# Kernel optimization log

Hardware: AMD Instinct MI355X
Metric: run time of the kernel (lower is better)

The kernel has to match this reference:

```python
import jax, jax.numpy as jnp
import numpy as np

NPOINT = 1024
K = 16
D_MODEL = 512
EPS = 1e-5


def _fps(xyz, npoint):
    # deterministic farthest point sampling (start at index 0)
    B, N, _ = xyz.shape
    def step(carry, _):
        dist, far = carry                                   # [B,N], [B]
        cent = jnp.take_along_axis(xyz, far[:, None, None], axis=1)  # [B,1,3]
        d = jnp.sum((xyz - cent) ** 2, axis=-1)             # [B,N]
        dist = jnp.minimum(dist, d)
        nxt = jnp.argmax(dist, axis=-1).astype(jnp.int32)
        return (dist, nxt), far
    init = (jnp.full((B, N), 1e10, xyz.dtype), jnp.zeros((B,), jnp.int32))
    _, idx = jax.lax.scan(step, init, None, length=npoint)
    return jnp.transpose(idx)                                # [B, npoint]


def _bn_relu(x, gamma, beta):
    # BatchNorm (training-mode batch stats, biased var) over all axes but channel-last
    axes = tuple(range(x.ndim - 1))
    mu = jnp.mean(x, axes, keepdims=True)
    var = jnp.var(x, axes, keepdims=True)
    return jax.nn.relu((x - mu) * jax.lax.rsqrt(var + EPS) * gamma + beta)


def _forward(xyz, feat, w1, b1, g1, bt1, fc1_w, fc1_b, wq, wk, wv, fc2_w, fc2_b,
             w2, b2, g2, bt2):
    B, N, C = feat.shape
    fps_idx = _fps(xyz, NPOINT)                              # [B,S]
    new_xyz = jnp.take_along_axis(xyz, fps_idx[:, :, None], axis=1)  # [B,S,3]
    # kNN of sampled centers against all points: squared distances [B,S,N]
    d = (jnp.sum(new_xyz ** 2, -1)[:, :, None]
         + jnp.sum(xyz ** 2, -1)[:, None, :]
         - 2.0 * jnp.einsum('bsc,bnc->bsn', new_xyz, xyz))
    _, knn_idx = jax.lax.top_k(-d, K)                        # [B,S,K]
    grouped = jnp.take_along_axis(
        feat, knn_idx.reshape(B, -1)[:, :, None], axis=1
    ).reshape(B, NPOINT, K, C)                               # [B,S,K,C]
    # mlp1: 1x1 conv + BN + ReLU (channel-last)
    x = _bn_relu(grouped @ w1.T + b1, g1, bt1)
    # TransformerBlock: local self-attention over the K neighbors
    pre = x
    h = x @ fc1_w.T + fc1_b                                  # [B,S,K,D]
    q, kk, v = h @ wq.T, h @ wk.T, h @ wv.T
    attn = jax.nn.softmax(
        jnp.einsum('bsnd,bsmd->bsnm', q, kk) / np.sqrt(D_MODEL), axis=-1)
    res = jnp.einsum('bsnm,bsmd->bsnd', attn, v)
    x = res @ fc2_w.T + fc2_b + pre                          # [B,S,K,C]
    # mlp2: 1x1 conv + BN + ReLU -> out_channel
    x = _bn_relu(x @ w2.T + b2, g2, bt2)                     # [B,S,K,out]
    new_feat = jnp.max(x, axis=2)                            # max-pool over neighbors
    return new_xyz, new_feat


def setup_inputs() -> dict:
    key = jax.random.key(0)
    ks = jax.random.split(key, 12)
    s = 0.02
    return {
        'xyz': jax.random.uniform(ks[0], (8, 4096, 3), jnp.float32),
        'feat': jax.random.normal(ks[1], (8, 4096, 64), jnp.float32),
        'w1': jax.random.normal(ks[2], (64, 64), jnp.float32) * s,
        'b1': jnp.zeros((64,), jnp.float32),
        'g1': jnp.ones((64,), jnp.float32),
        'bt1': jnp.zeros((64,), jnp.float32),
        'fc1_w': jax.random.normal(ks[3], (512, 64), jnp.float32) * s,
        'fc1_b': jnp.zeros((512,), jnp.float32),
        'wq': jax.random.normal(ks[4], (512, 512), jnp.float32) * s,
        'wk': jax.random.normal(ks[5], (512, 512), jnp.float32) * s,
        'wv': jax.random.normal(ks[6], (512, 512), jnp.float32) * s,
        'fc2_w': jax.random.normal(ks[7], (64, 512), jnp.float32) * s,
        'fc2_b': jnp.zeros((64,), jnp.float32),
        'w2': jax.random.normal(ks[8], (128, 64), jnp.float32) * s,
        'b2': jnp.zeros((128,), jnp.float32),
        'g2': jnp.ones((128,), jnp.float32),
        'bt2': jnp.zeros((128,), jnp.float32),
    }


def reference(xyz, feat, w1, b1, g1, bt1, fc1_w, fc1_b, wq, wk, wv, fc2_w, fc2_b,
              w2, b2, g2, bt2):
    return _forward(xyz, feat, w1, b1, g1, bt1, fc1_w, fc1_b, wq, wk, wv,
                    fc2_w, fc2_b, w2, b2, g2, bt2)
```

## Files before the change

### kernel.cpp

```cpp
#include <hip/hip_runtime.h>

#define EPSBN 1e-5f
#define INVSQ 0.04419417382415922f

#define WS_KNN_IDX   32768u
#define WS_X1        1048576u
#define WS_BNP1      34603008u
#define WS_BN1S      34865152u
#define WS_BNP2      34865664u
#define WS_BN2S      35914240u
#define WS_A         35915264u
#define WS_B         36046336u
#define WS_QB        36177408u
#define WS_KB        36179456u
#define WS_WC        36181504u
#define WS_G         36312576u
#define WS_ZT        36328960u
#define WS_U         36345344u
#define WS_W         36345600u
#define WS_TB        36345856u
#define WS_CC        36346112u
#define WS_PTS4      36346368u

__global__ __launch_bounds__(256) void prep1_kernel(const float* __restrict__ wq,
                                                    const float* __restrict__ wk,
                                                    const float* __restrict__ fc1w,
                                                    const float* __restrict__ fc1b,
                                                    const float* __restrict__ fc2w,
                                                    const float* __restrict__ wv,
                                                    const float* __restrict__ xyz,
                                                    float* __restrict__ A, float* __restrict__ B,
                                                    float* __restrict__ qb, float* __restrict__ kb,
                                                    float* __restrict__ Wc,
                                                    float4* __restrict__ pts4) {
  const int blk = blockIdx.x;
  if (blk < 256) {
    int id = blk * 256 + threadIdx.x;
    int which = id >> 15;
    int rem = id & 32767;
    int r = rem >> 6, i = rem & 63;
    const float* W = which ? wk : wq;
    float s = 0.f;
    for (int d = 0; d < 512; ++d) s = fmaf(W[r * 512 + d], fc1w[d * 64 + i], s);
    (which ? B : A)[r * 64 + i] = s;
    if (i == 0) {
      float sb = 0.f;
      for (int d = 0; d < 512; ++d) sb = fmaf(W[r * 512 + d], fc1b[d], sb);
      (which ? kb : qb)[r] = sb;
    }
  } else if (blk < 384) {
    int id = (blk - 256) * 256 + threadIdx.x;
    int c = id >> 9, d = id & 511;
    float s = 0.f;
    for (int e = 0; e < 512; ++e) s = fmaf(fc2w[c * 512 + e], wv[e * 512 + d], s);
    Wc[c * 512 + d] = s;
  } else {
    int id = (blk - 384) * 256 + threadIdx.x;
    float x = xyz[id * 3 + 0], y = xyz[id * 3 + 1], z = xyz[id * 3 + 2];
    float pp = __fadd_rn(__fadd_rn(__fmul_rn(x, x), __fmul_rn(y, y)), __fmul_rn(z, z));
    pts4[id] = make_float4(x, y, z, pp);
  }
}

#define FPS_REDSTEP(CTRL)                                                              \
  {                                                                                    \
    unsigned lo2 = (unsigned)__builtin_amdgcn_update_dpp(0, (int)klo, CTRL, 0xF, 0xF, true); \
    unsigned hi2 = (unsigned)__builtin_amdgcn_update_dpp(0, (int)khi, CTRL, 0xF, 0xF, true); \
    bool tk = (hi2 > khi) || (hi2 == khi && lo2 > klo);                                \
    khi = tk ? hi2 : khi; klo = tk ? lo2 : klo;                                        \
  }

__global__ __launch_bounds__(256) void fps_prep2_kernel(
    const float4* __restrict__ pts4, float* __restrict__ out_xyz,
    const float* __restrict__ A, const float* __restrict__ B,
    const float* __restrict__ qb, const float* __restrict__ kb,
    const float* __restrict__ Wc, const float* __restrict__ fc1w,
    const float* __restrict__ fc1b, const float* __restrict__ fc2b,
    float* __restrict__ G, float* __restrict__ u, float* __restrict__ w,
    float* __restrict__ cc, float* __restrict__ ZT, float* __restrict__ tb) {
  if (blockIdx.x >= 8) {
    const int blk = blockIdx.x - 8;
    if (blk < 17) {
      int id = blk * 256 + threadIdx.x;
      if (id < 4096) {
        int i = id >> 6, j = id & 63;
        float s = 0.f;
        for (int d = 0; d < 512; ++d) s = fmaf(A[d * 64 + i], B[d * 64 + j], s);
        G[i * 64 + j] = s * INVSQ;
      } else if (id < 4160) {
        int i = id - 4096; float s = 0.f;
        for (int d = 0; d < 512; ++d) s = fmaf(A[d * 64 + i], kb[d], s);
        u[i] = s * INVSQ;
      } else if (id < 4224) {
        int j = id - 4160; float s = 0.f;
        for (int d = 0; d < 512; ++d) s = fmaf(B[d * 64 + j], qb[d], s);
        w[j] = s * INVSQ;
      } else if (id == 4224) {
        float s = 0.f;
        for (int d = 0; d < 512; ++d) s = fmaf(qb[d], kb[d], s);
        cc[0] = s * INVSQ;
      }
    } else {
      int id = (blk - 17) * 256 + threadIdx.x;
      if (id < 4096) {
        int i = id >> 6, c = id & 63;
        float s = 0.f;
        for (int d = 0; d < 512; ++d) s = fmaf(Wc[c * 512 + d], fc1w[d * 64 + i], s);
        ZT[i * 64 + c] = s;
      } else if (id < 4160) {
        int c = id - 4096; float s = 0.f;
        for (int d = 0; d < 512; ++d) s = fmaf(Wc[c * 512 + d], fc1b[d], s);
        tb[c] = s + fc2b[c];
      }
    }
    return;
  }
  __shared__ float4 spts[4096];
  __shared__ float4 cent4[1024];
  __shared__ unsigned long long red[2][4];
  const int b = blockIdx.x;
  const int t = threadIdx.x;
  const int lane = t & 63, wid = t >> 6;
  const float4* pb = pts4 + (size_t)b * 4096;
  float px[16], py[16], pz[16], pd[16];
#pragma unroll
  for (int i = 0; i < 16; ++i) {
    int j = i * 256 + t;
    float4 p = pb[j];
    spts[j] = p;
    px[i] = p.x; py[i] = p.y; pz[i] = p.z; pd[i] = 1e10f;
  }
  __syncthreads();
  float4 c4 = spts[0];
  for (int it = 0; it < 1024; ++it) {
    if (t == 0) cent4[it] = c4;
    float bv = -1.0f; int bj = 0;
#pragma unroll
    for (int i = 0; i < 16; ++i) {
      float dx = __fsub_rn(px[i], c4.x);
      float dy = __fsub_rn(py[i], c4.y);
      float dz = __fsub_rn(pz[i], c4.z);
      float d = __fadd_rn(__fadd_rn(__fmul_rn(dx, dx), __fmul_rn(dy, dy)), __fmul_rn(dz, dz));
      float nd = fminf(pd[i], d);
      pd[i] = nd;
      bool g = nd > bv;
      bv = g ? nd : bv;
      bj = g ? (i * 256 + t) : bj;
    }
    unsigned klo = 4095u - (unsigned)bj;
    unsigned khi = __float_as_uint(bv);
    FPS_REDSTEP(0x111)
    FPS_REDSTEP(0x112)
    FPS_REDSTEP(0x114)
    FPS_REDSTEP(0x118)
    FPS_REDSTEP(0x142)
    FPS_REDSTEP(0x143)
    unsigned wlo = (unsigned)__builtin_amdgcn_readlane((int)klo, 63);
    unsigned whi = (unsigned)__builtin_amdgcn_readlane((int)khi, 63);
    const int par = it & 1;
    if (lane == 0) red[par][wid] = (((unsigned long long)whi) << 32) | wlo;
    __syncthreads();
    const ulonglong2* r2 = reinterpret_cast<const ulonglong2*>(&red[par][0]);
    ulonglong2 ka = r2[0];
    ulonglong2 kb2 = r2[1];
    unsigned long long m0 = (ka.x > ka.y) ? ka.x : ka.y;
    unsigned long long m1 = (kb2.x > kb2.y) ? kb2.x : kb2.y;
    unsigned long long k0 = (m0 > m1) ? m0 : m1;
    int jw = 4095 - (int)(unsigned)(k0 & 0xFFFFFFFFull);
    c4 = spts[jw];
  }
  __syncthreads();
  for (int o = t; o < 3072; o += 256) {
    int j = o / 3;
    int c = o - 3 * j;
    out_xyz[(size_t)b * 3072 + o] = (&cent4[j].x)[c];
  }
}

__global__ __launch_bounds__(256) void knn_kernel(const float4* __restrict__ pts4,
                                                  const float* __restrict__ new_xyz,
                                                  int* __restrict__ knn_idx) {
  const int t = threadIdx.x & 63;
  const int wave = (blockIdx.x << 2) | (threadIdx.x >> 6);
  const int b = wave >> 10;
  const float4* P = pts4 + (size_t)b * 4096;
  const float cx = new_xyz[(size_t)wave * 3 + 0];
  const float cy = new_xyz[(size_t)wave * 3 + 1];
  const float cz = new_xyz[(size_t)wave * 3 + 2];
  const float cc = __fadd_rn(__fadd_rn(__fmul_rn(cx, cx), __fmul_rn(cy, cy)), __fmul_rn(cz, cz));
  float ldd[16]; int ldi[16];
#pragma unroll
  for (int q = 0; q < 16; ++q) { ldd[q] = 3.4e38f; ldi[q] = 0x7fffffff; }
  for (int i = 0; i < 64; ++i) {
    int j = i * 64 + t;
    float4 p = P[j];
    float dot = __fadd_rn(__fadd_rn(__fmul_rn(cx, p.x), __fmul_rn(cy, p.y)), __fmul_rn(cz, p.z));
    float d = __fsub_rn(__fadd_rn(cc, p.w), __fmul_rn(2.0f, dot));
    if (d < ldd[15] || (d == ldd[15] && j < ldi[15])) {
      float cd = d; int ci = j;
#pragma unroll
      for (int q = 0; q < 16; ++q) {
        bool sw = (cd < ldd[q]) || (cd == ldd[q] && ci < ldi[q]);
        float td = ldd[q]; int ti = ldi[q];
        if (sw) { ldd[q] = cd; ldi[q] = ci; cd = td; ci = ti; }
      }
    }
  }
  float cd = ldd[0]; int ci = ldi[0];
  int* op = knn_idx + (size_t)wave * 16;
#pragma unroll 1
  for (int k = 0; k < 16; ++k) {
    float wd = cd; int wi = ci;
#pragma unroll
    for (int off = 1; off < 64; off <<= 1) {
      float ov = __shfl_xor(wd, off);
      int   oi = __shfl_xor(wi, off);
      bool tk = (ov < wd) || (ov == wd && oi < wi);
      wd = tk ? ov : wd; wi = tk ? oi : wi;
    }
    if (t == 0) op[k] = wi;
    if (wd == cd && wi == ci) {
#pragma unroll
      for (int q = 0; q < 15; ++q) { ldd[q] = ldd[q + 1]; ldi[q] = ldi[q + 1]; }
      ldd[15] = 3.4e38f; ldi[15] = 0x7fffffff;
    }
    cd = ldd[0]; ci = ldi[0];
  }
}

__global__ __launch_bounds__(256) void mlp1_kernel(const float* __restrict__ feat,
                                                   const int* __restrict__ knn_idx,
                                                   const float* __restrict__ w1,
                                                   const float* __restrict__ b1,
                                                   float* __restrict__ x1,
                                                   float* __restrict__ bnp1) {
  __shared__ float w1s[64 * 64];
  __shared__ float b1s[64];
  __shared__ float ls[4][64], lq[4][64];
  const int t = threadIdx.x;
  for (int i = t; i < 4096; i += 256) w1s[i] = w1[i];
  if (t < 64) b1s[t] = b1[t];
  __syncthreads();
  const int pos = blockIdx.x * 256 + t;
  const int b = pos >> 14;
  const int n = knn_idx[pos];
  const float4* fp = reinterpret_cast<const float4*>(feat + ((size_t)(b * 4096 + n)) * 64);
  float4 fr[16];
#pragma unroll
  for (int i = 0; i < 16; ++i) fr[i] = fp[i];
  float4* op = reinterpret_cast<float4*>(x1 + (size_t)pos * 64);
#pragma unroll
  for (int cq = 0; cq < 16; ++cq) {
    float a0 = b1s[cq * 4 + 0], a1 = b1s[cq * 4 + 1], a2 = b1s[cq * 4 + 2], a3 = b1s[cq * 4 + 3];
#pragma unroll
    for (int iq = 0; iq < 16; ++iq) {
      float4 f4 = fr[iq];
      float4 wa = *reinterpret_cast<const float4*>(&w1s[(cq * 4 + 0) * 64 + iq * 4]);
      float4 wb = *reinterpret_cast<const float4*>(&w1s[(cq * 4 + 1) * 64 + iq * 4]);
      float4 wc = *reinterpret_cast<const float4*>(&w1s[(cq * 4 + 2) * 64 + iq * 4]);
      float4 wd = *reinterpret_cast<const float4*>(&w1s[(cq * 4 + 3) * 64 + iq * 4]);
      a0 += f4.x * wa.x + f4.y * wa.y + f4.z * wa.z + f4.w * wa.w;
      a1 += f4.x * wb.x + f4.y * wb.y + f4.z * wb.z + f4.w * wb.w;
      a2 += f4.x * wc.x + f4.y * wc.y + f4.z * wc.z + f4.w * wc.w;
      a3 += f4.x * wd.x + f4.y * wd.y + f4.z * wd.z + f4.w * wd.w;
    }
    op[cq] = make_float4(a0, a1, a2, a3);
  }
  __threadfence_block();
  __syncthreads();
  {
    const int c2 = t & 63, g = t >> 6;
    const float* p = x1 + ((size_t)blockIdx.x * 256 + g * 64) * 64 + c2;
    float s = 0.f, s2 = 0.f;
    for (int i = 0; i < 64; ++i) { float v = p[(size_t)i * 64]; s += v; s2 = fmaf(v, v, s2); }
    ls[g][c2] = s; lq[g][c2] = s2;
  }
  __syncthreads();
  if (t < 64) {
    bnp1[blockIdx.x * 128 + t]      = ls[0][t] + ls[1][t] + ls[2][t] + ls[3][t];
    bnp1[blockIdx.x * 128 + 64 + t] = lq[0][t] + lq[1][t] + lq[2][t] + lq[3][t];
  }
}

__global__ __launch_bounds__(256) void bn1_final_kernel(const float* __restrict__ bnp1,
                                                        const float* __restrict__ g1,
                                                        const float* __restrict__ bt1,
                                                        float* __restrict__ bn1s) {
  __shared__ float rs[4][64], rq[4][64];
  const int t = threadIdx.x, c = t & 63, g = t >> 6;
  float S = 0.f, Q = 0.f;
  for (int i = g * 128; i < g * 128 + 128; ++i) {
    S += bnp1[i * 128 + c];
    Q += bnp1[i * 128 + 64 + c];
  }
  rs[g][c] = S; rq[g][c] = Q;
  __syncthreads();
  if (t < 64) {
    float Sa = rs[0][t] + rs[1][t] + rs[2][t] + rs[3][t];
    float Qa = rq[0][t] + rq[1][t] + rq[2][t] + rq[3][t];
    float m = Sa * (1.0f / 131072.0f);
    float var = Qa * (1.0f / 131072.0f) - m * m;
    float sc = g1[t] * rsqrtf(var + EPSBN);
    bn1s[t] = sc;
    bn1s[64 + t] = bt1[t] - m * sc;
  }
}

__global__ __launch_bounds__(64) void transformer_fused(
    float* __restrict__ x1, const float* __restrict__ bn1s,
    const float* __restrict__ G, const float* __restrict__ u, const float* __restrict__ w,
    const float* __restrict__ cc, const float* __restrict__ ZT, const float* __restrict__ tb) {
  __shared__ float pre[16][65];
  __shared__ float ts[16][65];
  __shared__ float ys[16][65];
  __shared__ float ss[16][17];
  __shared__ float spu[16], spw[16];
  const int c = threadIdx.x;
  const size_t base = (size_t)blockIdx.x * 1024;
  const float sc = bn1s[c], sh = bn1s[64 + c];
  float pc[16];
#pragma unroll
  for (int k = 0; k < 16; ++k) {
    float v = x1[base + k * 64 + c];
    float p = fmaxf(0.f, v * sc + sh);
    pc[k] = p; pre[k][c] = p;
  }
  __syncthreads();
  float tcol[16], ycol[16];
#pragma unroll
  for (int k = 0; k < 16; ++k) { tcol[k] = 0.f; ycol[k] = 0.f; }
  for (int i = 0; i < 64; ++i) {
    float g = G[i * 64 + c];
    float z = ZT[i * 64 + c];
#pragma unroll
    for (int k = 0; k < 16; ++k) {
      float p = pre[k][i];
      tcol[k] = fmaf(p, g, tcol[k]);
      ycol[k] = fmaf(p, z, ycol[k]);
    }
  }
#pragma unroll
  for (int k = 0; k < 16; ++k) { ts[k][c] = tcol[k]; ys[k][c] = ycol[k]; }
  if (c < 16) {
    float s = 0.f;
    for (int i = 0; i < 64; ++i) s = fmaf(pre[c][i], u[i], s);
    spu[c] = s;
  } else if (c < 32) {
    int m = c - 16; float s = 0.f;
    for (int i = 0; i < 64; ++i) s = fmaf(pre[m][i], w[i], s);
    spw[m] = s;
  }
  __syncthreads();
  {
    const float cval = cc[0];
    const int m = c & 15, nb = c >> 4;
#pragma unroll
    for (int ng = 0; ng < 4; ++ng) {
      int n = ng * 4 + nb;
      float s = 0.f;
      for (int i = 0; i < 64; ++i) s = fmaf(ts[n][i], pre[m][i], s);
      ss[n][m] = s + spu[n] + spw[m] + cval;
    }
  }
  __syncthreads();
  if (c < 16) {
    float mx = -3.4e38f;
#pragma unroll
    for (int m = 0; m < 16; ++m) mx = fmaxf(mx, ss[c][m]);
    float e[16], sum = 0.f;
#pragma unroll
    for (int m = 0; m < 16; ++m) { e[m] = expf(ss[c][m] - mx); sum += e[m]; }
    float r = 1.0f / sum;
#pragma unroll
    for (int m = 0; m < 16; ++m) ss[c][m] = e[m] * r;
  }
  __syncthreads();
  const float tbc = tb[c];
  float o[16];
#pragma unroll
  for (int k = 0; k < 16; ++k) o[k] = 0.f;
#pragma unroll
  for (int m = 0; m < 16; ++m) {
    float yv = ys[m][c];
#pragma unroll
    for (int k = 0; k < 16; ++k) o[k] = fmaf(ss[k][m], yv, o[k]);
  }
#pragma unroll
  for (int k = 0; k < 16; ++k) x1[base + k * 64 + c] = o[k] + tbc + pc[k];
}

__global__ __launch_bounds__(256) void bn2_stats_kernel(const float* __restrict__ x2,
                                                        const float* __restrict__ w2,
                                                        const float* __restrict__ b2,
                                                        float* __restrict__ bnp2,
                                                        float* __restrict__ out) {
  __shared__ float sx2[128 * 64];
  __shared__ float ps[2][128], pq[2][128];
  const int t = threadIdx.x;
  const float4* s4 = reinterpret_cast<const float4*>(x2 + (size_t)blockIdx.x * 128 * 64);
  float4* d4 = reinterpret_cast<float4*>(sx2);
  for (int i = 0; i < 8; ++i) d4[i * 256 + t] = s4[i * 256 + t];
  __syncthreads();
  const int c = t & 127, h = t >> 7;
  float4 wreg[16];
  const float4* w4 = reinterpret_cast<const float4*>(w2 + c * 64);
#pragma unroll
  for (int i = 0; i < 16; ++i) wreg[i] = w4[i];
  const float bb = b2[c];
  float s = 0.f, q = 0.f;
  float* omax = out + 24576 + ((size_t)blockIdx.x * 8 + 4 * h) * 128 + c;
#pragma unroll
  for (int gi = 0; gi < 4; ++gi) {
    float mx = -3.4e38f;
#pragma unroll 4
    for (int p2 = 0; p2 < 16; ++p2) {
      const int p = gi * 16 + p2;
      const float4* xr = reinterpret_cast<const float4*>(&sx2[(h * 64 + p) * 64]);
      float acc = bb;
#pragma unroll
      for (int i = 0; i < 16; ++i) {
        float4 xv = xr[i];
        acc += xv.x * wreg[i].x + xv.y * wreg[i].y + xv.z * wreg[i].z + xv.w * wreg[i].w;
      }
      s += acc; q = fmaf(acc, acc, q);
      mx = fmaxf(mx, acc);
    }
    omax[(size_t)gi * 128] = mx;
  }
  ps[h][c] = s; pq[h][c] = q;
  __syncthreads();
  if (t < 128) {
    bnp2[blockIdx.x * 256 + t]       = ps[0][t] + ps[1][t];
    bnp2[blockIdx.x * 256 + 128 + t] = pq[0][t] + pq[1][t];
  }
}

__global__ __launch_bounds__(512) void bn2_final_kernel(const float* __restrict__ bnp2,
                                                        const float* __restrict__ g2,
                                                        const float* __restrict__ bt2,
                                                        float* __restrict__ bn2s) {
  __shared__ float rs[4][128], rq[4][128];
  const int t = threadIdx.x, c = t & 127, g = t >> 7;
  float S = 0.f, Q = 0.f;
  for (int i = g * 256; i < g * 256 + 256; ++i) {
    S += bnp2[i * 256 + c];
    Q += bnp2[i * 256 + 128 + c];
  }
  rs[g][c] = S; rq[g][c] = Q;
  __syncthreads();
  if (t < 128) {
    float Sa = rs[0][t] + rs[1][t] + rs[2][t] + rs[3][t];
    float Qa = rq[0][t] + rq[1][t] + rq[2][t] + rq[3][t];
    float m = Sa * (1.0f / 131072.0f);
    float var = Qa * (1.0f / 131072.0f) - m * m;
    float sc = g2[t] * rsqrtf(var + EPSBN);
    bn2s[t] = sc;
    bn2s[128 + t] = bt2[t] - m * sc;
  }
}

__global__ __launch_bounds__(256) void final_kernel(const float* __restrict__ bn2s,
                                                    float* __restrict__ out) {
  __shared__ float s_sc[128], s_sh[128];
  const int t = threadIdx.x;
  if (t < 128) { s_sc[t] = bn2s[t]; s_sh[t] = bn2s[128 + t]; }
  __syncthreads();
  const int base = blockIdx.x * 1024 + t;
#pragma unroll
  for (int r = 0; r < 4; ++r) {
    const int i = base + r * 256;
    const int c = i & 127;
    float v = out[24576 + i];
    out[24576 + i] = fmaxf(0.f, v * s_sc[c] + s_sh[c]);
  }
}

extern "C" void kernel_launch(void* const* d_in, const int* in_sizes, int n_in,
                              void* d_out, int out_size, void* d_ws, size_t ws_size,
                              hipStream_t stream) {
  const float* xyz  = (const float*)d_in[0];
  const float* feat = (const float*)d_in[1];
  const float* w1   = (const float*)d_in[2];
  const float* b1   = (const float*)d_in[3];
  const float* g1   = (const float*)d_in[4];
  const float* bt1  = (const float*)d_in[5];
  const float* fc1w = (const float*)d_in[6];
  const float* fc1b = (const float*)d_in[7];
  const float* wq   = (const float*)d_in[8];
  const float* wk   = (const float*)d_in[9];
  const float* wv   = (const float*)d_in[10];
  const float* fc2w = (const float*)d_in[11];
  const float* fc2b = (const float*)d_in[12];
  const float* w2   = (const float*)d_in[13];
  const float* b2   = (const float*)d_in[14];
  const float* g2   = (const float*)d_in[15];
  const float* bt2  = (const float*)d_in[16];
  float* out = (float*)d_out;
  char* ws = (char*)d_ws;

  int*    knn_idx = (int*)(ws + WS_KNN_IDX);
  float*  x1      = (float*)(ws + WS_X1);
  float*  bnp1    = (float*)(ws + WS_BNP1);
  float*  bn1s    = (float*)(ws + WS_BN1S);
  float*  bnp2    = (float*)(ws + WS_BNP2);
  float*  bn2s    = (float*)(ws + WS_BN2S);
  float*  Abuf    = (float*)(ws + WS_A);
  float*  Bbuf    = (float*)(ws + WS_B);
  float*  qb      = (float*)(ws + WS_QB);
  float*  kb      = (float*)(ws + WS_KB);
  float*  Wc      = (float*)(ws + WS_WC);
  float*  G       = (float*)(ws + WS_G);
  float*  ZT      = (float*)(ws + WS_ZT);
  float*  u       = (float*)(ws + WS_U);
  float*  w       = (float*)(ws + WS_W);
  float*  tb      = (float*)(ws + WS_TB);
  float*  cc      = (float*)(ws + WS_CC);
  float4* pts4    = (float4*)(ws + WS_PTS4);

  prep1_kernel<<<512, 256, 0, stream>>>(wq, wk, fc1w, fc1b, fc2w, wv, xyz,
                                        Abuf, Bbuf, qb, kb, Wc, pts4);
  fps_prep2_kernel<<<42, 256, 0, stream>>>(pts4, out, Abuf, Bbuf, qb, kb, Wc,
                                           fc1w, fc1b, fc2b, G, u, w, cc, ZT, tb);
  knn_kernel<<<2048, 256, 0, stream>>>(pts4, out, knn_idx);
  mlp1_kernel<<<512, 256, 0, stream>>>(feat, knn_idx, w1, b1, x1, bnp1);
  bn1_final_kernel<<<1, 256, 0, stream>>>(bnp1, g1, bt1, bn1s);
  transformer_fused<<<8192, 64, 0, stream>>>(x1, bn1s, G, u, w, cc, ZT, tb);
  bn2_stats_kernel<<<1024, 256, 0, stream>>>(x1, w2, b2, bnp2, out);
  bn2_final_kernel<<<1, 512, 0, stream>>>(bnp2, g2, bt2, bn2s);
  final_kernel<<<1024, 256, 0, stream>>>(bn2s, out);
}
```

Before: 1.287 ms.

## Pipeline FPS in chunks with overlapped kNN and MLP1 stages

```diff
diff --git a/kernel.cpp b/kernel.cpp
--- a/kernel.cpp
+++ b/kernel.cpp
@@ -21,6 +21,8 @@
 #define WS_TB        36345856u
 #define WS_CC        36346112u
 #define WS_PTS4      36346368u
+#define WS_FPSPD     36870656u
+#define WS_FPSC4     37001728u
 
 __global__ __launch_bounds__(256) void prep1_kernel(const float* __restrict__ wq,
                                                     const float* __restrict__ wk,
@@ -70,14 +72,95 @@
     khi = tk ? hi2 : khi; klo = tk ? lo2 : klo;                                        \
   }
 
+__device__ __forceinline__ void fps_chunk_body(unsigned char* smem, const float4* __restrict__ pts4,
+                                               float* __restrict__ out_xyz,
+                                               float* __restrict__ fps_pd,
+                                               float4* __restrict__ fps_c4,
+                                               int it0, int b, int t) {
+  float4* spts = reinterpret_cast<float4*>(smem);
+  float4* cent = reinterpret_cast<float4*>(smem + 65536);
+  unsigned long long* red = reinterpret_cast<unsigned long long*>(smem + 69632);
+  const int lane = t & 63, wid = t >> 6;
+  const float4* pb = pts4 + (size_t)b * 4096;
+  float px[16], py[16], pz[16], pd[16];
+  if (it0 == 0) {
+#pragma unroll
+    for (int i = 0; i < 16; ++i) {
+      int j = i * 256 + t;
+      float4 p = pb[j];
+      spts[j] = p;
+      px[i] = p.x; py[i] = p.y; pz[i] = p.z; pd[i] = 1e10f;
+    }
+  } else {
+#pragma unroll
+    for (int i = 0; i < 16; ++i) {
+      int j = i * 256 + t;
+      float4 p = pb[j];
+      spts[j] = p;
+      px[i] = p.x; py[i] = p.y; pz[i] = p.z;
+      pd[i] = fps_pd[i * 2048 + b * 256 + t];
+    }
+  }
+  __syncthreads();
+  float4 c4 = (it0 == 0) ? spts[0] : fps_c4[b];
+  for (int it = it0; it < it0 + 256; ++it) {
+    if (t == 0) cent[it - it0] = c4;
+    float bv = -1.0f; int bj = 0;
+#pragma unroll
+    for (int i = 0; i < 16; ++i) {
+      float dx = __fsub_rn(px[i], c4.x);
+      float dy = __fsub_rn(py[i], c4.y);
+      float dz = __fsub_rn(pz[i], c4.z);
+      float d = __fadd_rn(__fadd_rn(__fmul_rn(dx, dx), __fmul_rn(dy, dy)), __fmul_rn(dz, dz));
+      float nd = fminf(pd[i], d);
+      pd[i] = nd;
+      bool g = nd > bv;
+      bv = g ? nd : bv;
+      bj = g ? (i * 256 + t) : bj;
+    }
+    unsigned klo = 4095u - (unsigned)bj;
+    unsigned khi = __float_as_uint(bv);
+    FPS_REDSTEP(0x111)
+    FPS_REDSTEP(0x112)
+    FPS_REDSTEP(0x114)
+    FPS_REDSTEP(0x118)
+    FPS_REDSTEP(0x142)
+    FPS_REDSTEP(0x143)
+    unsigned wlo = (unsigned)__builtin_amdgcn_readlane((int)klo, 63);
+    unsigned whi = (unsigned)__builtin_amdgcn_readlane((int)khi, 63);
+    const int par = it & 1;
+    if (lane == 0) red[par * 4 + wid] = (((unsigned long long)whi) << 32) | wlo;
+    __syncthreads();
+    const ulonglong2* r2 = reinterpret_cast<const ulonglong2*>(&red[par * 4]);
+    ulonglong2 ka = r2[0];
+    ulonglong2 kb2 = r2[1];
+    unsigned long long m0 = (ka.x > ka.y) ? ka.x : ka.y;
+    unsigned long long m1 = (kb2.x > kb2.y) ? kb2.x : kb2.y;
+    unsigned long long k0 = (m0 > m1) ? m0 : m1;
+    int jw = 4095 - (int)(unsigned)(k0 & 0xFFFFFFFFull);
+    c4 = spts[jw];
+  }
+#pragma unroll
+  for (int i = 0; i < 16; ++i) fps_pd[i * 2048 + b * 256 + t] = pd[i];
+  if (t == 0) fps_c4[b] = c4;
+  __syncthreads();
+  for (int o = t; o < 768; o += 256) {
+    int j = o / 3;
+    int c = o - 3 * j;
+    out_xyz[(size_t)b * 3072 + (size_t)it0 * 3 + o] = (&cent[j].x)[c];
+  }
+}
+
 __global__ __launch_bounds__(256) void fps_prep2_kernel(
     const float4* __restrict__ pts4, float* __restrict__ out_xyz,
+    float* __restrict__ fps_pd, float4* __restrict__ fps_c4,
     const float* __restrict__ A, const float* __restrict__ B,
     const float* __restrict__ qb, const float* __restrict__ kb,
     const float* __restrict__ Wc, const float* __restrict__ fc1w,
     const float* __restrict__ fc1b, const float* __restrict__ fc2b,
     float* __restrict__ G, float* __restrict__ u, float* __restrict__ w,
     float* __restrict__ cc, float* __restrict__ ZT, float* __restrict__ tb) {
+  __shared__ __align__(16) unsigned char smem[69696];
   if (blockIdx.x >= 8) {
     const int blk = blockIdx.x - 8;
     if (blk < 17) {
@@ -115,170 +198,130 @@
     }
     return;
   }
-  __shared__ float4 spts[4096];
-  __shared__ float4 cent4[1024];
-  __shared__ unsigned long long red[2][4];
-  const int b = blockIdx.x;
+  fps_chunk_body(smem, pts4, out_xyz, fps_pd, fps_c4, 0, blockIdx.x, threadIdx.x);
+}
+
+__global__ __launch_bounds__(256) void pipe_kernel(
+    const float4* __restrict__ pts4, float* __restrict__ out_xyz,
+    float* __restrict__ fps_pd, float4* __restrict__ fps_c4,
+    int it0, int knn_c0, int mlp_c0,
+    int* __restrict__ knn_idx,
+    const float* __restrict__ feat, const float* __restrict__ w1,
+    const float* __restrict__ b1, float* __restrict__ x1, float* __restrict__ bnp1) {
+  __shared__ __align__(16) unsigned char smem[69696];
   const int t = threadIdx.x;
-  const int lane = t & 63, wid = t >> 6;
-  const float4* pb = pts4 + (size_t)b * 4096;
-  float px[16], py[16], pz[16], pd[16];
-#pragma unroll
-  for (int i = 0; i < 16; ++i) {
-    int j = i * 256 + t;
-    float4 p = pb[j];
-    spts[j] = p;
-    px[i] = p.x; py[i] = p.y; pz[i] = p.z; pd[i] = 1e10f;
-  }
-  __syncthreads();
-  float4 c4 = spts[0];
-  for (int it = 0; it < 1024; ++it) {
-    if (t == 0) cent4[it] = c4;
-    float bv = -1.0f; int bj = 0;
-#pragma unroll
-    for (int i = 0; i < 16; ++i) {
-      float dx = __fsub_rn(px[i], c4.x);
-      float dy = __fsub_rn(py[i], c4.y);
-      float dz = __fsub_rn(pz[i], c4.z);
-      float d = __fadd_rn(__fadd_rn(__fmul_rn(dx, dx), __fmul_rn(dy, dy)), __fmul_rn(dz, dz));
-      float nd = fminf(pd[i], d);
-      pd[i] = nd;
-      bool g = nd > bv;
-      bv = g ? nd : bv;
-      bj = g ? (i * 256 + t) : bj;
-    }
-    unsigned klo = 4095u - (unsigned)bj;
-    unsigned khi = __float_as_uint(bv);
-    FPS_REDSTEP(0x111)
-    FPS_REDSTEP(0x112)
-    FPS_REDSTEP(0x114)
-    FPS_REDSTEP(0x118)
-    FPS_REDSTEP(0x142)
-    FPS_REDSTEP(0x143)
-    unsigned wlo = (unsigned)__builtin_amdgcn_readlane((int)klo, 63);
-    unsigned whi = (unsigned)__builtin_amdgcn_readlane((int)khi, 63);
-    const int par = it & 1;
-    if (lane == 0) red[par][wid] = (((unsigned long long)whi) << 32) | wlo;
+  int base = 0;
+  if (it0 >= 0) {
+    if (blockIdx.x < 8) {
+      fps_chunk_body(smem, pts4, out_xyz, fps_pd, fps_c4, it0, blockIdx.x, t);
+      return;
+    }
+    base = 8;
+  }
+  if (knn_c0 >= 0) {
+    if ((int)blockIdx.x < base + 512) {
+      const int blk = blockIdx.x - base;
+      const int lane = t & 63;
+      const int wv = (blk << 2) | (t >> 6);
+      const int b = wv >> 8;
+      const int center = b * 1024 + knn_c0 + (wv & 255);
+      const float4* P = pts4 + (size_t)b * 4096;
+      const float cx = out_xyz[(size_t)center * 3 + 0];
+      const float cy = out_xyz[(size_t)center * 3 + 1];
+      const float cz = out_xyz[(size_t)center * 3 + 2];
+      const float cc = __fadd_rn(__fadd_rn(__fmul_rn(cx, cx), __fmul_rn(cy, cy)), __fmul_rn(cz, cz));
+      float ldd[16]; int ldi[16];
+#pragma unroll
+      for (int q = 0; q < 16; ++q) { ldd[q] = 3.4e38f; ldi[q] = 0x7fffffff; }
+      for (int i = 0; i < 64; ++i) {
+        int j = i * 64 + lane;
+        float4 p = P[j];
+        float dot = __fadd_rn(__fadd_rn(__fmul_rn(cx, p.x), __fmul_rn(cy, p.y)), __fmul_rn(cz, p.z));
+        float d = __fsub_rn(__fadd_rn(cc, p.w), __fmul_rn(2.0f, dot));
+        if (d < ldd[15] || (d == ldd[15] && j < ldi[15])) {
+          float cd = d; int ci = j;
+#pragma unroll
+          for (int q = 0; q < 16; ++q) {
+            bool sw = (cd < ldd[q]) || (cd == ldd[q] && ci < ldi[q]);
+            float td = ldd[q]; int ti = ldi[q];
+            if (sw) { ldd[q] = cd; ldi[q] = ci; cd = td; ci = ti; }
+          }
+        }
+      }
+      float cd = ldd[0]; int ci = ldi[0];
+      int* op = knn_idx + (size_t)center * 16;
+#pragma unroll 1
+      for (int k = 0; k < 16; ++k) {
+        float wd = cd; int wi = ci;
+#pragma unroll
+        for (int off = 1; off < 64; off <<= 1) {
+          float ov = __shfl_xor(wd, off);
+          int   oi = __shfl_xor(wi, off);
+          bool tk = (ov < wd) || (ov == wd && oi < wi);
+          wd = tk ? ov : wd; wi = tk ? oi : wi;
+        }
+        if (lane == 0) op[k] = wi;
+        if (wd == cd && wi == ci) {
+#pragma unroll
+          for (int q = 0; q < 15; ++q) { ldd[q] = ldd[q + 1]; ldi[q] = ldi[q + 1]; }
+          ldd[15] = 3.4e38f; ldi[15] = 0x7fffffff;
+        }
+        cd = ldd[0]; ci = ldi[0];
+      }
+      return;
+    }
+    base += 512;
+  }
+  {
+    const int blk = blockIdx.x - base;
+    float* w1s = reinterpret_cast<float*>(smem);
+    float* b1s = reinterpret_cast<float*>(smem + 16384);
+    float (*ls)[64] = reinterpret_cast<float(*)[64]>(smem + 16640);
+    float (*lq)[64] = reinterpret_cast<float(*)[64]>(smem + 17664);
+    for (int i = t; i < 4096; i += 256) w1s[i] = w1[i];
+    if (t < 64) b1s[t] = b1[t];
     __syncthreads();
-    const ulonglong2* r2 = reinterpret_cast<const ulonglong2*>(&red[par][0]);
-    ulonglong2 ka = r2[0];
-    ulonglong2 kb2 = r2[1];
-    unsigned long long m0 = (ka.x > ka.y) ? ka.x : ka.y;
-    unsigned long long m1 = (kb2.x > kb2.y) ? kb2.x : kb2.y;
-    unsigned long long k0 = (m0 > m1) ? m0 : m1;
-    int jw = 4095 - (int)(unsigned)(k0 & 0xFFFFFFFFull);
-    c4 = spts[jw];
-  }
-  __syncthreads();
-  for (int o = t; o < 3072; o += 256) {
-    int j = o / 3;
-    int c = o - 3 * j;
-    out_xyz[(size_t)b * 3072 + o] = (&cent4[j].x)[c];
-  }
-}
-
-__global__ __launch_bounds__(256) void knn_kernel(const float4* __restrict__ pts4,
-                                                  const float* __restrict__ new_xyz,
-                                                  int* __restrict__ knn_idx) {
-  const int t = threadIdx.x & 63;
-  const int wave = (blockIdx.x << 2) | (threadIdx.x >> 6);
-  const int b = wave >> 10;
-  const float4* P = pts4 + (size_t)b * 4096;
-  const float cx = new_xyz[(size_t)wave * 3 + 0];
-  const float cy = new_xyz[(size_t)wave * 3 + 1];
-  const float cz = new_xyz[(size_t)wave * 3 + 2];
-  const float cc = __fadd_rn(__fadd_rn(__fmul_rn(cx, cx), __fmul_rn(cy, cy)), __fmul_rn(cz, cz));
-  float ldd[16]; int ldi[16];
-#pragma unroll
-  for (int q = 0; q < 16; ++q) { ldd[q] = 3.4e38f; ldi[q] = 0x7fffffff; }
-  for (int i = 0; i < 64; ++i) {
-    int j = i * 64 + t;
-    float4 p = P[j];
-    float dot = __fadd_rn(__fadd_rn(__fmul_rn(cx, p.x), __fmul_rn(cy, p.y)), __fmul_rn(cz, p.z));
-    float d = __fsub_rn(__fadd_rn(cc, p.w), __fmul_rn(2.0f, dot));
-    if (d < ldd[15] || (d == ldd[15] && j < ldi[15])) {
-      float cd = d; int ci = j;
-#pragma unroll
-      for (int q = 0; q < 16; ++q) {
-        bool sw = (cd < ldd[q]) || (cd == ldd[q] && ci < ldi[q]);
-        float td = ldd[q]; int ti = ldi[q];
-        if (sw) { ldd[q] = cd; ldi[q] = ci; cd = td; ci = ti; }
+    const int batch = blk >> 4;
+    const size_t pbase = ((size_t)batch * 1024 + mlp_c0 + (blk & 15) * 16) * 16;
+    const size_t pos = pbase + t;
+    const int n = knn_idx[pos];
+    const float4* fp = reinterpret_cast<const float4*>(feat + ((size_t)(batch * 4096 + n)) * 64);
+    float4 fr[16];
+#pragma unroll
+    for (int i = 0; i < 16; ++i) fr[i] = fp[i];
+    float4* op = reinterpret_cast<float4*>(x1 + pos * 64);
+#pragma unroll
+    for (int cq = 0; cq < 16; ++cq) {
+      float a0 = b1s[cq * 4 + 0], a1 = b1s[cq * 4 + 1], a2 = b1s[cq * 4 + 2], a3 = b1s[cq * 4 + 3];
+#pragma unroll
+      for (int iq = 0; iq < 16; ++iq) {
+        float4 f4 = fr[iq];
+        float4 wa = *reinterpret_cast<const float4*>(&w1s[(cq * 4 + 0) * 64 + iq * 4]);
+        float4 wb = *reinterpret_cast<const float4*>(&w1s[(cq * 4 + 1) * 64 + iq * 4]);
+        float4 wc = *reinterpret_cast<const float4*>(&w1s[(cq * 4 + 2) * 64 + iq * 4]);
+        float4 wd = *reinterpret_cast<const float4*>(&w1s[(cq * 4 + 3) * 64 + iq * 4]);
+        a0 += f4.x * wa.x + f4.y * wa.y + f4.z * wa.z + f4.w * wa.w;
+        a1 += f4.x * wb.x + f4.y * wb.y + f4.z * wb.z + f4.w * wb.w;
+        a2 += f4.x * wc.x + f4.y * wc.y + f4.z * wc.z + f4.w * wc.w;
+        a3 += f4.x * wd.x + f4.y * wd.y + f4.z * wd.z + f4.w * wd.w;
       }
-    }
-  }
-  float cd = ldd[0]; int ci = ldi[0];
-  int* op = knn_idx + (size_t)wave * 16;
-#pragma unroll 1
-  for (int k = 0; k < 16; ++k) {
-    float wd = cd; int wi = ci;
-#pragma unroll
-    for (int off = 1; off < 64; off <<= 1) {
-      float ov = __shfl_xor(wd, off);
-      int   oi = __shfl_xor(wi, off);
-      bool tk = (ov < wd) || (ov == wd && oi < wi);
-      wd = tk ? ov : wd; wi = tk ? oi : wi;
-    }
-    if (t == 0) op[k] = wi;
-    if (wd == cd && wi == ci) {
-#pragma unroll
-      for (int q = 0; q < 15; ++q) { ldd[q] = ldd[q + 1]; ldi[q] = ldi[q + 1]; }
-      ldd[15] = 3.4e38f; ldi[15] = 0x7fffffff;
-    }
-    cd = ldd[0]; ci = ldi[0];
-  }
-}
-
-__global__ __launch_bounds__(256) void mlp1_kernel(const float* __restrict__ feat,
-                                                   const int* __restrict__ knn_idx,
-                                                   const float* __restrict__ w1,
-                                                   const float* __restrict__ b1,
-                                                   float* __restrict__ x1,
-                                                   float* __restrict__ bnp1) {
-  __shared__ float w1s[64 * 64];
-  __shared__ float b1s[64];
-  __shared__ float ls[4][64], lq[4][64];
-  const int t = threadIdx.x;
-  for (int i = t; i < 4096; i += 256) w1s[i] = w1[i];
-  if (t < 64) b1s[t] = b1[t];
-  __syncthreads();
-  const int pos = blockIdx.x * 256 + t;
-  const int b = pos >> 14;
-  const int n = knn_idx[pos];
-  const float4* fp = reinterpret_cast<const float4*>(feat + ((size_t)(b * 4096 + n)) * 64);
-  float4 fr[16];
-#pragma unroll
-  for (int i = 0; i < 16; ++i) fr[i] = fp[i];
-  float4* op = reinterpret_cast<float4*>(x1 + (size_t)pos * 64);
-#pragma unroll
-  for (int cq = 0; cq < 16; ++cq) {
-    float a0 = b1s[cq * 4 + 0], a1 = b1s[cq * 4 + 1], a2 = b1s[cq * 4 + 2], a3 = b1s[cq * 4 + 3];
-#pragma unroll
-    for (int iq = 0; iq < 16; ++iq) {
-      float4 f4 = fr[iq];
-      float4 wa = *reinterpret_cast<const float4*>(&w1s[(cq * 4 + 0) * 64 + iq * 4]);
-      float4 wb = *reinterpret_cast<const float4*>(&w1s[(cq * 4 + 1) * 64 + iq * 4]);
-      float4 wc = *reinterpret_cast<const float4*>(&w1s[(cq * 4 + 2) * 64 + iq * 4]);
-      float4 wd = *reinterpret_cast<const float4*>(&w1s[(cq * 4 + 3) * 64 + iq * 4]);
-      a0 += f4.x * wa.x + f4.y * wa.y + f4.z * wa.z + f4.w * wa.w;
-      a1 += f4.x * wb.x + f4.y * wb.y + f4.z * wb.z + f4.w * wb.w;
-      a2 += f4.x * wc.x + f4.y * wc.y + f4.z * wc.z + f4.w * wc.w;
-      a3 += f4.x * wd.x + f4.y * wd.y + f4.z * wd.z + f4.w * wd.w;
-    }
-    op[cq] = make_float4(a0, a1, a2, a3);
-  }
-  __threadfence_block();
-  __syncthreads();
-  {
-    const int c2 = t & 63, g = t >> 6;
-    const float* p = x1 + ((size_t)blockIdx.x * 256 + g * 64) * 64 + c2;
-    float s = 0.f, s2 = 0.f;
-    for (int i = 0; i < 64; ++i) { float v = p[(size_t)i * 64]; s += v; s2 = fmaf(v, v, s2); }
-    ls[g][c2] = s; lq[g][c2] = s2;
-  }
-  __syncthreads();
-  if (t < 64) {
-    bnp1[blockIdx.x * 128 + t]      = ls[0][t] + ls[1][t] + ls[2][t] + ls[3][t];
-    bnp1[blockIdx.x * 128 + 64 + t] = lq[0][t] + lq[1][t] + lq[2][t] + lq[3][t];
+      op[cq] = make_float4(a0, a1, a2, a3);
+    }
+    __threadfence_block();
+    __syncthreads();
+    {
+      const int c2 = t & 63, g = t >> 6;
+      const float* p = x1 + (pbase + g * 64) * 64 + c2;
+      float s = 0.f, s2 = 0.f;
+      for (int i = 0; i < 64; ++i) { float v = p[(size_t)i * 64]; s += v; s2 = fmaf(v, v, s2); }
+      ls[g][c2] = s; lq[g][c2] = s2;
+    }
+    __syncthreads();
+    if (t < 64) {
+      const int slot = (mlp_c0 >> 8) * 128 + blk;
+      bnp1[slot * 128 + t]      = ls[0][t] + ls[1][t] + ls[2][t] + ls[3][t];
+      bnp1[slot * 128 + 64 + t] = lq[0][t] + lq[1][t] + lq[2][t] + lq[3][t];
+    }
   }
 }
 
@@ -516,13 +559,24 @@
   float*  tb      = (float*)(ws + WS_TB);
   float*  cc      = (float*)(ws + WS_CC);
   float4* pts4    = (float4*)(ws + WS_PTS4);
+  float*  fps_pd  = (float*)(ws + WS_FPSPD);
+  float4* fps_c4  = (float4*)(ws + WS_FPSC4);
 
   prep1_kernel<<<512, 256, 0, stream>>>(wq, wk, fc1w, fc1b, fc2w, wv, xyz,
                                         Abuf, Bbuf, qb, kb, Wc, pts4);
-  fps_prep2_kernel<<<42, 256, 0, stream>>>(pts4, out, Abuf, Bbuf, qb, kb, Wc,
+  fps_prep2_kernel<<<42, 256, 0, stream>>>(pts4, out, fps_pd, fps_c4,
+                                           Abuf, Bbuf, qb, kb, Wc,
                                            fc1w, fc1b, fc2b, G, u, w, cc, ZT, tb);
-  knn_kernel<<<2048, 256, 0, stream>>>(pts4, out, knn_idx);
-  mlp1_kernel<<<512, 256, 0, stream>>>(feat, knn_idx, w1, b1, x1, bnp1);
+  pipe_kernel<<<520, 256, 0, stream>>>(pts4, out, fps_pd, fps_c4, 256, 0, -1,
+                                       knn_idx, feat, w1, b1, x1, bnp1);
+  pipe_kernel<<<648, 256, 0, stream>>>(pts4, out, fps_pd, fps_c4, 512, 256, 0,
+                                       knn_idx, feat, w1, b1, x1, bnp1);
+  pipe_kernel<<<648, 256, 0, stream>>>(pts4, out, fps_pd, fps_c4, 768, 512, 256,
+                                       knn_idx, feat, w1, b1, x1, bnp1);
+  pipe_kernel<<<640, 256, 0, stream>>>(pts4, out, fps_pd, fps_c4, -1, 768, 512,
+                                       knn_idx, feat, w1, b1, x1, bnp1);
+  pipe_kernel<<<128, 256, 0, stream>>>(pts4, out, fps_pd, fps_c4, -1, -1, 768,
+                                       knn_idx, feat, w1, b1, x1, bnp1);
   bn1_final_kernel<<<1, 256, 0, stream>>>(bnp1, g1, bt1, bn1s);
   transformer_fused<<<8192, 64, 0, stream>>>(x1, bn1s, G, u, w, cc, ZT, tb);
   bn2_stats_kernel<<<1024, 256, 0, stream>>>(x1, w2, b2, bnp2, out);
```

Measured after the change: 1.194 ms. 1.08x faster.
